# Kernel tuning notes

Measured on AMD Instinct MI355X. Metric: run time of the kernel, lower is better.

The kernel has to match this reference:

```python
import jax, jax.numpy as jnp
import numpy as np

N = 16384
E = 262144
HID = 128
NFILT = 128
NGAUSS = 50
NINTER = 6
CUTOFF = 10.0
NUMZ = 100
LOG2 = 0.6931471805599453


def ssp(x):
    # ShiftedSoftplus
    return jax.nn.softplus(x) - LOG2


def setup_inputs() -> dict:
    key = jax.random.key(0)
    ks = jax.random.split(key, 20)
    z = jax.random.randint(ks[0], (N,), 0, NUMZ)
    pos = jax.random.uniform(ks[1], (N, 3), dtype=jnp.float32) * 5.0  # box side 5 -> all pairs < cutoff
    edge_index = jax.random.randint(ks[2], (2, E), 0, N)
    s = lambda k, shape, fan: jax.random.normal(k, shape, dtype=jnp.float32) / np.sqrt(fan)
    params = dict(
        emb=s(ks[3], (NUMZ, HID), 1.0),
        Wf1=s(ks[4], (NINTER, NGAUSS, NFILT), NGAUSS), bf1=jnp.zeros((NINTER, NFILT), jnp.float32),
        Wf2=s(ks[5], (NINTER, NFILT, NFILT), NFILT), bf2=jnp.zeros((NINTER, NFILT), jnp.float32),
        Wl1=s(ks[6], (NINTER, HID, NFILT), HID),
        Wl2=s(ks[7], (NINTER, NFILT, HID), NFILT), bl2=jnp.zeros((NINTER, HID), jnp.float32),
        Wl=s(ks[8], (NINTER, HID, HID), HID), bl=jnp.zeros((NINTER, HID), jnp.float32),
        Wo1=s(ks[9], (HID, HID // 2), HID), bo1=jnp.zeros((HID // 2,), jnp.float32),
        Wo2=s(ks[10], (HID // 2, 1), HID // 2), bo2=jnp.zeros((1,), jnp.float32),
    )
    return dict(z=z, pos=pos, edge_index=edge_index, **params)


def reference(z, pos, edge_index, emb, Wf1, bf1, Wf2, bf2, Wl1, Wl2, bl2, Wl, bl, Wo1, bo1, Wo2, bo2):
    src, dst = edge_index[0], edge_index[1]
    # edge distances and Gaussian smearing
    d = jnp.linalg.norm(pos[src] - pos[dst], axis=-1)          # [E]
    offset = jnp.linspace(0.0, CUTOFF, NGAUSS, dtype=jnp.float32)
    coeff = -0.5 / (offset[1] - offset[0]) ** 2
    ea = jnp.exp(coeff * (d[:, None] - offset) ** 2)            # [E, NGAUSS]
    C = 0.5 * (jnp.cos(d * (np.pi / CUTOFF)) + 1.0)             # cosine cutoff [E]

    h = emb[z]                                                  # [N, HID]
    for i in range(NINTER):
        # continuous-filter weights
        Wfilt = (ssp(ea @ Wf1[i] + bf1[i]) @ Wf2[i] + bf2[i]) * C[:, None]  # [E, NFILT]
        x = h @ Wl1[i]                                          # lin1, no bias [N, NFILT]
        msg = x[src] * Wfilt                                    # gather + filter
        agg = jax.ops.segment_sum(msg, dst, num_segments=N)     # scatter-sum [N, NFILT]
        x = ssp(agg @ Wl2[i] + bl2[i]) @ Wl[i] + bl[i]          # lin2 -> ssp -> lin
        h = h + x

    h = ssp(h @ Wo1 + bo1) @ Wo2 + bo2                          # [N, 1] per-atom energy
    out = jnp.sum(h, axis=0, keepdims=True)                     # 'add' readout, single graph -> [1, 1]
    return jax.nn.relu(out)
```

## Files before the change

### kernel.cpp

```cpp
#include <hip/hip_runtime.h>
#include <math.h>

#define NATOM 16384
#define NEDGE 262144
#define HID 128
#define NG 50
#define NI 6

typedef _Float16 h8_t __attribute__((ext_vector_type(8)));
typedef _Float16 h4_t __attribute__((ext_vector_type(4)));
typedef float    f4_t __attribute__((ext_vector_type(4)));

__device__ __forceinline__ float ssp_f(float v) {
    float e = __expf(-fabsf(v));
    return fmaxf(v, 0.0f) + __logf(1.0f + e) - 0.69314718055994531f;
}

__global__ void fill0(float* __restrict__ p, int n4) {
    int i = blockIdx.x * 256 + threadIdx.x;
    if (i < n4) ((float4*)p)[i] = make_float4(0.f, 0.f, 0.f, 0.f);
}

__global__ void hist_k(const int* __restrict__ ei, int* __restrict__ cnt) {
    int e = blockIdx.x * 256 + threadIdx.x;
    if (e < NEDGE) atomicAdd(&cnt[ei[NEDGE + e]], 1);
}

__global__ void scan_k(const int* __restrict__ cnt, int* __restrict__ offs) {
    __shared__ int part[256];
    int t = threadIdx.x;
    int base = t * 64;
    int s = 0;
    for (int i = 0; i < 64; ++i) s += cnt[base + i];
    part[t] = s;
    __syncthreads();
    for (int off = 1; off < 256; off <<= 1) {
        int v = (t >= off) ? part[t - off] : 0;
        __syncthreads();
        part[t] += v;
        __syncthreads();
    }
    int r = part[t] - s;
    for (int i = 0; i < 64; ++i) { offs[base + i] = r; r += cnt[base + i]; }
    if (t == 255) offs[NATOM] = r;
}

__global__ void scatter_k(const int* __restrict__ ei, const int* __restrict__ offs,
                          int* __restrict__ cnt, int* __restrict__ sSrc, int* __restrict__ sDst) {
    int e = blockIdx.x * 256 + threadIdx.x;
    if (e >= NEDGE) return;
    int d = ei[NEDGE + e];
    int r = atomicAdd(&cnt[d], 1);
    int j = offs[d] + r;
    sSrc[j] = ei[e];
    sDst[j] = d;
}

__global__ void edge_pre(const float* __restrict__ pos,
                         const int* __restrict__ sSrc, const int* __restrict__ sDst,
                         _Float16* __restrict__ ea, float* __restrict__ Cb) {
    int j = blockIdx.x * 256 + threadIdx.x;
    if (j >= NEDGE) return;
    int s = sSrc[j], dd = sDst[j];
    float dx = pos[3*s]   - pos[3*dd];
    float dy = pos[3*s+1] - pos[3*dd+1];
    float dz = pos[3*s+2] - pos[3*dd+2];
    float d = sqrtf(dx*dx + dy*dy + dz*dz);
    Cb[j] = 0.5f * (cosf(d * 0.31415926535897931f) + 1.0f);
    const float delta = 10.0f / 49.0f;
    const float coeff = -0.5f / (delta * delta);
    #pragma unroll
    for (int gq = 0; gq < 8; ++gq) {
        h8_t hv;
        #pragma unroll
        for (int r = 0; r < 8; ++r) {
            int g = gq * 8 + r;
            float v = 0.0f;
            if (g < NG) { float u = d - (float)g * delta; v = __expf(coeff * u * u); }
            hv[r] = (_Float16)v;
        }
        *(h8_t*)&ea[(size_t)j * 64 + gq * 8] = hv;
    }
}

__global__ void wprep(const float* __restrict__ Wf1, const float* __restrict__ Wf2,
                      const float* __restrict__ Wl1, const float* __restrict__ Wl2,
                      const float* __restrict__ Wl,
                      _Float16* __restrict__ w1, _Float16* __restrict__ w2,
                      _Float16* __restrict__ wn) {
    int idx = blockIdx.x * 256 + threadIdx.x;
    const int S1 = NI * 128 * 64, S2 = NI * 128 * 128;
    if (idx < S1) {
        int i = idx >> 13, r = idx & 8191, fo = r >> 6, k = r & 63;
        float v = (k < NG) ? Wf1[(size_t)i * NG * 128 + k * 128 + fo] : 0.0f;
        w1[idx] = (_Float16)v;
        return;
    }
    idx -= S1;
    if (idx < S2) {
        int i = idx >> 14, r = idx & 16383, fo = r >> 7, k = r & 127;
        w2[idx] = (_Float16)Wf2[(size_t)i * 128 * 128 + k * 128 + fo];
        return;
    }
    idx -= S2;
    if (idx < 3 * S2) {
        int mi = idx >> 14;
        int r = idx & 16383, fo = r >> 7, k = r & 127;
        int m = mi / NI, i = mi % NI;
        const float* W = (m == 0) ? Wl1 : (m == 1) ? Wl2 : Wl;
        wn[idx] = (_Float16)W[(size_t)i * 128 * 128 + k * 128 + fo];
    }
}

__global__ void embed_k(const int* __restrict__ z, const float* __restrict__ emb,
                        float* __restrict__ h) {
    int tid = blockIdx.x * 256 + threadIdx.x;
    int n = tid >> 7, f = tid & 127;
    h[tid] = emb[z[n] * HID + f];
}

__launch_bounds__(256)
__global__ void gemm_node_mfma(const float* __restrict__ A,
                               const _Float16* __restrict__ wt,
                               _Float16* __restrict__ xh) {
    __shared__ _Float16 aS[64 * 136];
    int t = threadIdx.x;
    int mb = blockIdx.x * 64;
    #pragma unroll
    for (int j = 0; j < 8; ++j) {
        int idx = t + j * 256;
        int row = idx >> 5, c4 = idx & 31;
        f4_t v = *(const f4_t*)&A[(size_t)(mb + row) * HID + c4 * 4];
        h4_t hh;
        #pragma unroll
        for (int r = 0; r < 4; ++r) hh[r] = (_Float16)v[r];
        *(h4_t*)&aS[row * 136 + c4 * 4] = hh;
    }
    __syncthreads();

    int wv = t >> 6, lane = t & 63, l15 = lane & 15, quad = lane >> 4;
    f4_t acc[2][4];
    #pragma unroll
    for (int m = 0; m < 2; ++m)
        #pragma unroll
        for (int n = 0; n < 4; ++n) acc[m][n] = (f4_t)0.0f;

    for (int kc = 0; kc < 4; ++kc) {
        int k0 = kc * 32 + quad * 8;
        h8_t a[2];
        #pragma unroll
        for (int m = 0; m < 2; ++m)
            a[m] = *(const h8_t*)&wt[(wv * 32 + m * 16 + l15) * 128 + k0];
        #pragma unroll
        for (int n = 0; n < 4; ++n) {
            h8_t b = *(const h8_t*)&aS[(n * 16 + l15) * 136 + k0];
            #pragma unroll
            for (int m = 0; m < 2; ++m)
                acc[m][n] = __builtin_amdgcn_mfma_f32_16x16x32_f16(a[m], b, acc[m][n], 0, 0, 0);
        }
    }

    #pragma unroll
    for (int n = 0; n < 4; ++n) {
        int el = n * 16 + l15;
        size_t row = (size_t)(mb + el);
        #pragma unroll
        for (int m = 0; m < 2; ++m) {
            int fb = wv * 32 + m * 16 + quad * 4;
            h4_t o;
            #pragma unroll
            for (int r = 0; r < 4; ++r) o[r] = (_Float16)acc[m][n][r];
            *(h4_t*)&xh[row * 128 + fb] = o;
        }
    }
}

__launch_bounds__(256)
__global__ void gemm_node3(const float* __restrict__ agg,
                           const _Float16* __restrict__ w2t, const _Float16* __restrict__ wlt,
                           const _Float16* __restrict__ w1n,
                           const float* __restrict__ bl2, const float* __restrict__ bl,
                           float* __restrict__ h, _Float16* __restrict__ xh) {
    __shared__ _Float16 aS[32 * 136];
    int t = threadIdx.x;
    int mb = blockIdx.x * 32;
    #pragma unroll
    for (int j = 0; j < 4; ++j) {
        int idx = t + j * 256;
        int row = idx >> 5, c4 = idx & 31;
        f4_t v = *(const f4_t*)&agg[(size_t)(mb + row) * HID + c4 * 4];
        h4_t hh;
        #pragma unroll
        for (int r = 0; r < 4; ++r) hh[r] = (_Float16)v[r];
        *(h4_t*)&aS[row * 136 + c4 * 4] = hh;
    }
    __syncthreads();

    int wv = t >> 6, lane = t & 63, l15 = lane & 15, quad = lane >> 4;
    int fq = wv * 32 + quad * 4;
    f4_t acc[2][2];

    #pragma unroll
    for (int m = 0; m < 2; ++m)
        #pragma unroll
        for (int n = 0; n < 2; ++n) acc[m][n] = (f4_t)0.0f;
    for (int kc = 0; kc < 4; ++kc) {
        int k0 = kc * 32 + quad * 8;
        h8_t a[2];
        #pragma unroll
        for (int m = 0; m < 2; ++m)
            a[m] = *(const h8_t*)&w2t[(wv * 32 + m * 16 + l15) * 128 + k0];
        #pragma unroll
        for (int n = 0; n < 2; ++n) {
            h8_t b = *(const h8_t*)&aS[(n * 16 + l15) * 136 + k0];
            #pragma unroll
            for (int m = 0; m < 2; ++m)
                acc[m][n] = __builtin_amdgcn_mfma_f32_16x16x32_f16(a[m], b, acc[m][n], 0, 0, 0);
        }
    }
    f4_t b2v[2];
    b2v[0] = *(const f4_t*)&bl2[fq]; b2v[1] = *(const f4_t*)&bl2[fq + 16];
    __syncthreads();

    #pragma unroll
    for (int m = 0; m < 2; ++m)
        #pragma unroll
        for (int n = 0; n < 2; ++n) {
            int el = n * 16 + l15;
            int fb = wv * 32 + m * 16 + quad * 4;
            h4_t hh;
            #pragma unroll
            for (int r = 0; r < 4; ++r)
                hh[r] = (_Float16)ssp_f(acc[m][n][r] + b2v[m][r]);
            *(h4_t*)&aS[el * 136 + fb] = hh;
        }
    __syncthreads();

    #pragma unroll
    for (int m = 0; m < 2; ++m)
        #pragma unroll
        for (int n = 0; n < 2; ++n) acc[m][n] = (f4_t)0.0f;
    for (int kc = 0; kc < 4; ++kc) {
        int k0 = kc * 32 + quad * 8;
        h8_t a[2];
        #pragma unroll
        for (int m = 0; m < 2; ++m)
            a[m] = *(const h8_t*)&wlt[(wv * 32 + m * 16 + l15) * 128 + k0];
        #pragma unroll
        for (int n = 0; n < 2; ++n) {
            h8_t b = *(const h8_t*)&aS[(n * 16 + l15) * 136 + k0];
            #pragma unroll
            for (int m = 0; m < 2; ++m)
                acc[m][n] = __builtin_amdgcn_mfma_f32_16x16x32_f16(a[m], b, acc[m][n], 0, 0, 0);
        }
    }
    f4_t blv[2];
    blv[0] = *(const f4_t*)&bl[fq]; blv[1] = *(const f4_t*)&bl[fq + 16];
    __syncthreads();

    #pragma unroll
    for (int n = 0; n < 2; ++n) {
        int el = n * 16 + l15;
        size_t row = (size_t)(mb + el);
        #pragma unroll
        for (int m = 0; m < 2; ++m) {
            int fb = wv * 32 + m * 16 + quad * 4;
            f4_t hv = *(const f4_t*)&h[row * 128 + fb];
            f4_t o;
            h4_t hh;
            #pragma unroll
            for (int r = 0; r < 4; ++r) {
                o[r] = hv[r] + acc[m][n][r] + blv[m][r];
                hh[r] = (_Float16)o[r];
            }
            *(f4_t*)&h[row * 128 + fb] = o;
            *(h4_t*)&aS[el * 136 + fb] = hh;
        }
    }
    if (!w1n) return;
    __syncthreads();

    #pragma unroll
    for (int m = 0; m < 2; ++m)
        #pragma unroll
        for (int n = 0; n < 2; ++n) acc[m][n] = (f4_t)0.0f;
    for (int kc = 0; kc < 4; ++kc) {
        int k0 = kc * 32 + quad * 8;
        h8_t a[2];
        #pragma unroll
        for (int m = 0; m < 2; ++m)
            a[m] = *(const h8_t*)&w1n[(wv * 32 + m * 16 + l15) * 128 + k0];
        #pragma unroll
        for (int n = 0; n < 2; ++n) {
            h8_t b = *(const h8_t*)&aS[(n * 16 + l15) * 136 + k0];
            #pragma unroll
            for (int m = 0; m < 2; ++m)
                acc[m][n] = __builtin_amdgcn_mfma_f32_16x16x32_f16(a[m], b, acc[m][n], 0, 0, 0);
        }
    }
    #pragma unroll
    for (int n = 0; n < 2; ++n) {
        int el = n * 16 + l15;
        size_t row = (size_t)(mb + el);
        #pragma unroll
        for (int m = 0; m < 2; ++m) {
            int fb = wv * 32 + m * 16 + quad * 4;
            h4_t o;
            #pragma unroll
            for (int r = 0; r < 4; ++r) o[r] = (_Float16)acc[m][n][r];
            *(h4_t*)&xh[row * 128 + fb] = o;
        }
    }
}

#define T1_LDW 136
#define NDST 16

__launch_bounds__(256)
__global__ void edge_filter(const _Float16* __restrict__ xh, float* __restrict__ agg,
                            const int* __restrict__ sSrc, const int* __restrict__ sDst,
                            const int* __restrict__ offs, const float* __restrict__ Cb,
                            const _Float16* __restrict__ ea,
                            const _Float16* __restrict__ w1, const _Float16* __restrict__ w2,
                            const float* __restrict__ bf1, const float* __restrict__ bf2) {
    __shared__ __align__(16) _Float16 t1S[64 * T1_LDW];
    __shared__ float accS[NDST * 128];
    __shared__ int dstl[64];

    _Float16* msg = t1S;
    int t = threadIdx.x;
    int wv = t >> 6, lane = t & 63;
    int l15 = lane & 15, quad = lane >> 4;
    int d0 = blockIdx.x * NDST;
    int estart = offs[d0];
    int ecnt = offs[d0 + NDST] - estart;
    int tmax = (ecnt + 63) >> 6;

    #pragma unroll
    for (int c = 0; c < 2; ++c)
        *(f4_t*)&accS[(t + c * 256) * 4] = (f4_t)0.0f;

    h8_t w1f[2][2], w2f[4][2];
    #pragma unroll
    for (int kc = 0; kc < 2; ++kc) {
        int k0 = kc * 32 + quad * 8;
        #pragma unroll
        for (int m = 0; m < 2; ++m)
            w1f[kc][m] = *(const h8_t*)&w1[(wv * 32 + m * 16 + l15) * 64 + k0];
    }
    #pragma unroll
    for (int kc = 0; kc < 4; ++kc) {
        int k0 = kc * 32 + quad * 8;
        #pragma unroll
        for (int m = 0; m < 2; ++m)
            w2f[kc][m] = *(const h8_t*)&w2[(wv * 32 + m * 16 + l15) * 128 + k0];
    }
    int fq = wv * 32 + quad * 4;
    f4_t b1v[2], b2v[2];
    b1v[0] = *(const f4_t*)&bf1[fq];  b1v[1] = *(const f4_t*)&bf1[fq + 16];
    b2v[0] = *(const f4_t*)&bf2[fq];  b2v[1] = *(const f4_t*)&bf2[fq + 16];

    int srcn[4];
    float cn[4];
    #pragma unroll
    for (int n = 0; n < 4; ++n) {
        int rel = n * 16 + l15;
        bool ok = rel < ecnt;
        srcn[n] = ok ? sSrc[estart + rel] : 0;
        cn[n]   = ok ? Cb[estart + rel] : 0.0f;
    }

    for (int tt = 0; tt < tmax; ++tt) {
        int base = estart + tt * 64;
        int lim = ecnt - tt * 64;
        int limc = lim < 64 ? lim : 64;
        bool pre = (tt + 1 < tmax);

        int dln = 0;
        if (t < 64) dln = (t < limc) ? (sDst[base + t] - d0) : 0;

        int srcp[4];
        float cp[4];
        if (pre) {
            int base2 = base + 64, lim2 = lim - 64;
            #pragma unroll
            for (int n = 0; n < 4; ++n) {
                int rel = n * 16 + l15;
                bool ok = rel < lim2;
                srcp[n] = ok ? sSrc[base2 + rel] : 0;
                cp[n]   = ok ? Cb[base2 + rel] : 0.0f;
            }
        }

        h4_t xr[4][2];
        #pragma unroll
        for (int n = 0; n < 4; ++n)
            #pragma unroll
            for (int m = 0; m < 2; ++m)
                xr[n][m] = *(const h4_t*)&xh[(size_t)srcn[n] * HID + wv * 32 + m * 16 + quad * 4];

        f4_t acc1[2][4];
        #pragma unroll
        for (int m = 0; m < 2; ++m)
            #pragma unroll
            for (int n = 0; n < 4; ++n) acc1[m][n] = (f4_t)0.0f;
        #pragma unroll
        for (int kc = 0; kc < 2; ++kc) {
            int k0 = kc * 32 + quad * 8;
            h8_t b[4];
            #pragma unroll
            for (int n = 0; n < 4; ++n) {
                int rel = n * 16 + l15;
                int er = rel < limc ? rel : limc - 1;
                b[n] = *(const h8_t*)&ea[(size_t)(base + er) * 64 + k0];
            }
            #pragma unroll
            for (int m = 0; m < 2; ++m)
                #pragma unroll
                for (int n = 0; n < 4; ++n)
                    acc1[m][n] = __builtin_amdgcn_mfma_f32_16x16x32_f16(w1f[kc][m], b[n], acc1[m][n], 0, 0, 0);
        }

        #pragma unroll
        for (int m = 0; m < 2; ++m)
            #pragma unroll
            for (int n = 0; n < 4; ++n) {
                int el = n * 16 + l15;
                int fb = wv * 32 + m * 16 + quad * 4;
                h4_t hh;
                #pragma unroll
                for (int r = 0; r < 4; ++r)
                    hh[r] = (_Float16)ssp_f(acc1[m][n][r] + b1v[m][r]);
                *(h4_t*)&t1S[el * T1_LDW + fb] = hh;
            }
        __syncthreads();

        f4_t acc2[2][4];
        #pragma unroll
        for (int m = 0; m < 2; ++m)
            #pragma unroll
            for (int n = 0; n < 4; ++n) acc2[m][n] = (f4_t)0.0f;
        #pragma unroll
        for (int kc = 0; kc < 4; ++kc) {
            int k0 = kc * 32 + quad * 8;
            #pragma unroll
            for (int n = 0; n < 4; ++n) {
                h8_t b = *(const h8_t*)&t1S[(n * 16 + l15) * T1_LDW + k0];
                #pragma unroll
                for (int m = 0; m < 2; ++m)
                    acc2[m][n] = __builtin_amdgcn_mfma_f32_16x16x32_f16(w2f[kc][m], b, acc2[m][n], 0, 0, 0);
            }
        }
        __syncthreads();

        if (t < 64) dstl[t] = dln;
        #pragma unroll
        for (int n = 0; n < 4; ++n) {
            int el = n * 16 + l15;
            float ce = cn[n];
            #pragma unroll
            for (int m = 0; m < 2; ++m) {
                int fb = wv * 32 + m * 16 + quad * 4;
                h4_t o;
                #pragma unroll
                for (int r = 0; r < 4; ++r)
                    o[r] = (_Float16)((acc2[m][n][r] + b2v[m][r]) * ce * (float)xr[n][m][r]);
                *(h4_t*)&msg[el * T1_LDW + fb] = o;
            }
        }
        __syncthreads();

        {
            int fg = t & 15, rs = t >> 4;
            int f0 = fg * 8;
            int i0 = rs * 4;
            int4 dq = *(const int4*)&dstl[i0];
            int dd[4] = {dq.x, dq.y, dq.z, dq.w};
            float run[8];
            #pragma unroll
            for (int k = 0; k < 8; ++k) run[k] = 0.0f;
            int curd = dd[0];
            #pragma unroll
            for (int i = 0; i < 4; ++i) {
                int dnow = dd[i];
                if (dnow != curd) {
                    #pragma unroll
                    for (int k = 0; k < 8; ++k) atomicAdd(&accS[curd * 128 + f0 + k], run[k]);
                    #pragma unroll
                    for (int k = 0; k < 8; ++k) run[k] = 0.0f;
                    curd = dnow;
                }
                h8_t v = *(const h8_t*)&msg[(i0 + i) * T1_LDW + f0];
                #pragma unroll
                for (int k = 0; k < 8; ++k) run[k] += (float)v[k];
            }
            #pragma unroll
            for (int k = 0; k < 8; ++k) atomicAdd(&accS[curd * 128 + f0 + k], run[k]);
        }
        __syncthreads();

        if (pre) {
            #pragma unroll
            for (int n = 0; n < 4; ++n) { srcn[n] = srcp[n]; cn[n] = cp[n]; }
        }
    }

    float* dstp = &agg[(size_t)d0 * HID];
    #pragma unroll
    for (int c = 0; c < 2; ++c) {
        int idx = t + c * 256;
        *(f4_t*)&dstp[idx * 4] = *(const f4_t*)&accS[idx * 4];
    }
}

__launch_bounds__(256)
__global__ void readout1(const float* __restrict__ h, const float* __restrict__ Wo1,
                         const float* __restrict__ bo1, const float* __restrict__ Wo2,
                         const float* __restrict__ bo2, float* __restrict__ accum) {
    __shared__ float w1[128 * 64];
    __shared__ float part[4];
    int t = threadIdx.x;
    for (int i = t; i < 128 * 16; i += 256)
        ((float4*)w1)[i] = ((const float4*)Wo1)[i];
    __syncthreads();
    int f = t & 63, wv = t >> 6;
    float b = bo1[f], w2v = Wo2[f];
    float lsum = 0.0f;
    for (int a = 0; a < 16; ++a) {
        int n = blockIdx.x * 64 + wv * 16 + a;
        const float* hr = &h[(size_t)n * HID];
        float acc = b;
        #pragma unroll 16
        for (int k = 0; k < 128; ++k)
            acc = fmaf(hr[k], w1[k*64 + f], acc);
        lsum += ssp_f(acc) * w2v;
    }
    #pragma unroll
    for (int off = 32; off > 0; off >>= 1)
        lsum += __shfl_down(lsum, off, 64);
    if (f == 0) part[wv] = lsum;
    __syncthreads();
    if (t == 0)
        atomicAdd(accum, part[0] + part[1] + part[2] + part[3] + 64.0f * bo2[0]);
}

__global__ void readout2(const float* __restrict__ accum, float* __restrict__ out) {
    out[0] = fmaxf(accum[0], 0.0f);
}

extern "C" void kernel_launch(void* const* d_in, const int* in_sizes, int n_in,
                              void* d_out, int out_size, void* d_ws, size_t ws_size,
                              hipStream_t stream) {
    const int*   z   = (const int*)d_in[0];
    const float* pos = (const float*)d_in[1];
    const int*   ei  = (const int*)d_in[2];
    const float* emb = (const float*)d_in[3];
    const float* Wf1 = (const float*)d_in[4];
    const float* bf1 = (const float*)d_in[5];
    const float* Wf2 = (const float*)d_in[6];
    const float* bf2 = (const float*)d_in[7];
    const float* Wl1 = (const float*)d_in[8];
    const float* Wl2 = (const float*)d_in[9];
    const float* bl2 = (const float*)d_in[10];
    const float* Wl  = (const float*)d_in[11];
    const float* bl  = (const float*)d_in[12];
    const float* Wo1 = (const float*)d_in[13];
    const float* bo1 = (const float*)d_in[14];
    const float* Wo2 = (const float*)d_in[15];
    const float* bo2 = (const float*)d_in[16];
    float* out = (float*)d_out;

    _Float16* w1 = (_Float16*)d_ws;
    _Float16* w2 = w1 + NI * 8192;
    _Float16* wn = w2 + NI * 16384;
    _Float16* ea = wn + 3 * NI * 16384;
    _Float16* xh = ea + (size_t)NEDGE * 64;
    float* Cb  = (float*)(xh + (size_t)NATOM * 128);
    float* h   = Cb + NEDGE;
    float* agg = h + (size_t)NATOM * HID;
    float* accum = agg + (size_t)NATOM * HID;
    int* cnt  = (int*)(accum + 4);
    int* offs = cnt + NATOM;
    int* sSrc = offs + NATOM + 4;
    int* sDst = sSrc + NEDGE;

    fill0<<<NATOM/4/256, 256, 0, stream>>>((float*)cnt, NATOM/4);
    hist_k<<<NEDGE/256, 256, 0, stream>>>(ei, cnt);
    scan_k<<<1, 256, 0, stream>>>(cnt, offs);
    fill0<<<NATOM/4/256, 256, 0, stream>>>((float*)cnt, NATOM/4);
    scatter_k<<<NEDGE/256, 256, 0, stream>>>(ei, offs, cnt, sSrc, sDst);

    edge_pre<<<NEDGE/256, 256, 0, stream>>>(pos, sSrc, sDst, ea, Cb);
    wprep<<<(NI*8192 + NI*16384 + 3*NI*16384)/256, 256, 0, stream>>>(
        Wf1, Wf2, Wl1, Wl2, Wl, w1, w2, wn);
    embed_k<<<(NATOM*HID)/256, 256, 0, stream>>>(z, emb, h);

    gemm_node_mfma<<<NATOM/64, 256, 0, stream>>>(h, wn, xh);
    for (int i = 0; i < NI; ++i) {
        edge_filter<<<NATOM/NDST, 256, 0, stream>>>(xh, agg, sSrc, sDst, offs, Cb, ea,
            w1 + (size_t)i*8192, w2 + (size_t)i*16384,
            bf1 + i*HID, bf2 + i*HID);
        const _Float16* w1n = (i < NI-1) ? wn + (size_t)(i+1)*16384 : nullptr;
        gemm_node3<<<NATOM/32, 256, 0, stream>>>(agg,
            wn + (size_t)(1*NI+i)*16384, wn + (size_t)(2*NI+i)*16384,
            w1n, bl2 + i*HID, bl + i*HID, h, xh);
    }
    fill0<<<1, 256, 0, stream>>>(accum, 1);
    readout1<<<NATOM/64, 256, 0, stream>>>(h, Wo1, bo1, Wo2, bo2, accum);
    readout2<<<1, 1, 0, stream>>>(accum, out);
}
```

Baseline: 916.4 us.

## Stage edge-attribute tile in LDS, drop index prefetch, widen segmented reduction

The edge_filter kernel now copies each 64-edge Gaussian-feature tile into shared memory with coalesced loads, so the first MFMA reads its operands from LDS instead of doing strided global loads per wave. The software prefetch of next-tile src and cutoff values is removed; they are loaded at the top of each tile, which adds exposed latency. The segmented reduction now gives each thread one feature across 32 edges instead of 8 features across 4 edges, cutting shared atomics at the cost of a longer serial loop. The launch bounds add a minimum-occupancy hint and the kernel uses more LDS.

```diff
diff --git a/kernel.cpp b/kernel.cpp
--- a/kernel.cpp
+++ b/kernel.cpp
@@ -314,20 +314,23 @@
 }
 
 #define T1_LDW 136
+#define EA_LDW 72
 #define NDST 16
 
-__launch_bounds__(256)
+__launch_bounds__(256, 4)
 __global__ void edge_filter(const _Float16* __restrict__ xh, float* __restrict__ agg,
                             const int* __restrict__ sSrc, const int* __restrict__ sDst,
                             const int* __restrict__ offs, const float* __restrict__ Cb,
                             const _Float16* __restrict__ ea,
                             const _Float16* __restrict__ w1, const _Float16* __restrict__ w2,
                             const float* __restrict__ bf1, const float* __restrict__ bf2) {
+    __shared__ __align__(16) _Float16 eaS[64 * EA_LDW];
     __shared__ __align__(16) _Float16 t1S[64 * T1_LDW];
     __shared__ float accS[NDST * 128];
     __shared__ int dstl[64];
 
     _Float16* msg = t1S;
+
     int t = threadIdx.x;
     int wv = t >> 6, lane = t & 63;
     int l15 = lane & 15, quad = lane >> 4;
@@ -360,44 +363,39 @@
     b1v[0] = *(const f4_t*)&bf1[fq];  b1v[1] = *(const f4_t*)&bf1[fq + 16];
     b2v[0] = *(const f4_t*)&bf2[fq];  b2v[1] = *(const f4_t*)&bf2[fq + 16];
 
-    int srcn[4];
-    float cn[4];
-    #pragma unroll
-    for (int n = 0; n < 4; ++n) {
-        int rel = n * 16 + l15;
-        bool ok = rel < ecnt;
-        srcn[n] = ok ? sSrc[estart + rel] : 0;
-        cn[n]   = ok ? Cb[estart + rel] : 0.0f;
-    }
-
     for (int tt = 0; tt < tmax; ++tt) {
         int base = estart + tt * 64;
         int lim = ecnt - tt * 64;
-        int limc = lim < 64 ? lim : 64;
-        bool pre = (tt + 1 < tmax);
-
-        int dln = 0;
-        if (t < 64) dln = (t < limc) ? (sDst[base + t] - d0) : 0;
-
-        int srcp[4];
-        float cp[4];
-        if (pre) {
-            int base2 = base + 64, lim2 = lim - 64;
-            #pragma unroll
-            for (int n = 0; n < 4; ++n) {
-                int rel = n * 16 + l15;
-                bool ok = rel < lim2;
-                srcp[n] = ok ? sSrc[base2 + rel] : 0;
-                cp[n]   = ok ? Cb[base2 + rel] : 0.0f;
-            }
-        }
-
+
+        #pragma unroll
+        for (int c = 0; c < 2; ++c) {
+            int ch = t + c * 256;
+            int e = ch >> 3, ks = ch & 7;
+            h8_t v = (h8_t)(_Float16)0.0f;
+            if (e < lim) v = *(const h8_t*)&ea[(size_t)(base + e) * 64 + ks * 8];
+            *(h8_t*)&eaS[e * EA_LDW + ks * 8] = v;
+        }
+        if (t < 64) {
+            int dl = 0;
+            if (t < lim) dl = sDst[base + t] - d0;
+            dstl[t] = dl;
+        }
+        int srcn[4];
+        float cn[4];
+        #pragma unroll
+        for (int n = 0; n < 4; ++n) {
+            int rel = n * 16 + l15;
+            bool ok = rel < lim;
+            srcn[n] = ok ? sSrc[base + rel] : 0;
+            cn[n]   = ok ? Cb[base + rel] : 0.0f;
+        }
         h4_t xr[4][2];
         #pragma unroll
         for (int n = 0; n < 4; ++n)
             #pragma unroll
             for (int m = 0; m < 2; ++m)
                 xr[n][m] = *(const h4_t*)&xh[(size_t)srcn[n] * HID + wv * 32 + m * 16 + quad * 4];
+        __syncthreads();
 
         f4_t acc1[2][4];
         #pragma unroll
@@ -409,11 +407,8 @@
             int k0 = kc * 32 + quad * 8;
             h8_t b[4];
             #pragma unroll
-            for (int n = 0; n < 4; ++n) {
-                int rel = n * 16 + l15;
-                int er = rel < limc ? rel : limc - 1;
-                b[n] = *(const h8_t*)&ea[(size_t)(base + er) * 64 + k0];
-            }
+            for (int n = 0; n < 4; ++n)
+                b[n] = *(const h8_t*)&eaS[(n * 16 + l15) * EA_LDW + k0];
             #pragma unroll
             for (int m = 0; m < 2; ++m)
                 #pragma unroll
@@ -453,7 +448,6 @@
         }
         __syncthreads();
 
-        if (t < 64) dstl[t] = dln;
         #pragma unroll
         for (int n = 0; n < 4; ++n) {
             int el = n * 16 + l15;
@@ -471,38 +465,22 @@
         __syncthreads();
 
         {
-            int fg = t & 15, rs = t >> 4;
-            int f0 = fg * 8;
-            int i0 = rs * 4;
-            int4 dq = *(const int4*)&dstl[i0];
-            int dd[4] = {dq.x, dq.y, dq.z, dq.w};
-            float run[8];
-            #pragma unroll
-            for (int k = 0; k < 8; ++k) run[k] = 0.0f;
-            int curd = dd[0];
-            #pragma unroll
-            for (int i = 0; i < 4; ++i) {
-                int dnow = dd[i];
-                if (dnow != curd) {
-                    #pragma unroll
-                    for (int k = 0; k < 8; ++k) atomicAdd(&accS[curd * 128 + f0 + k], run[k]);
-                    #pragma unroll
-                    for (int k = 0; k < 8; ++k) run[k] = 0.0f;
-                    curd = dnow;
+            int f = t & 127, hf = t >> 7;
+            int ib = hf * 32;
+            float run = 0.0f;
+            int cur = dstl[ib];
+            for (int i = ib; i < ib + 32; ++i) {
+                int dnow = dstl[i];
+                if (dnow != cur) {
+                    atomicAdd(&accS[cur * 128 + f], run);
+                    run = 0.0f;
+                    cur = dnow;
                 }
-                h8_t v = *(const h8_t*)&msg[(i0 + i) * T1_LDW + f0];
-                #pragma unroll
-                for (int k = 0; k < 8; ++k) run[k] += (float)v[k];
+                run += (float)msg[i * T1_LDW + f];
             }
-            #pragma unroll
-            for (int k = 0; k < 8; ++k) atomicAdd(&accS[curd * 128 + f0 + k], run[k]);
-        }
-        __syncthreads();
-
-        if (pre) {
-            #pragma unroll
-            for (int n = 0; n < 4; ++n) { srcn[n] = srcp[n]; cn[n] = cp[n]; }
-        }
+            atomicAdd(&accS[cur * 128 + f], run);
+        }
+        __syncthreads();
     }
 
     float* dstp = &agg[(size_t)d0 * HID];
```

New measurement: 782.4 us. -14.6%, faster.
